# Optimization experiments

Hardware: AMD Instinct MI355X
Metric: run time of the kernel (lower is better)

The kernel has to match this reference:

```python
import jax, jax.numpy as jnp
import numpy as np

# --- hyperparameters (from MambaBlock init) ---
DIM = 256          # d_model per window
STEP = 128         # int(dim * hop), hop = 0.5
N_MAMBA = 2
D_STATE = 16
D_CONV = 4
EXPAND = 4
D_INNER = EXPAND * DIM          # 1024
DT_RANK = -(-DIM // 16)         # ceil(d_model/16) = 16
EPS = 1e-5
B_SZ = 4
T_LEN = 131072


def setup_inputs() -> dict:
    key = jax.random.key(0)
    ks = jax.random.split(key, 8)
    s = 0.02
    x = jax.random.normal(ks[0], (B_SZ, T_LEN), dtype=jnp.float32)
    in_proj_w = jax.random.normal(ks[1], (N_MAMBA, 2 * D_INNER, DIM), dtype=jnp.float32) * s
    conv_w = jax.random.normal(ks[2], (N_MAMBA, D_INNER, 1, D_CONV), dtype=jnp.float32) * 0.1
    conv_b = jnp.zeros((N_MAMBA, D_INNER), dtype=jnp.float32)
    x_proj_w = jax.random.normal(ks[3], (N_MAMBA, DT_RANK + 2 * D_STATE, D_INNER), dtype=jnp.float32) * s
    dt_std = DT_RANK ** -0.5
    dt_proj_w = jax.random.uniform(ks[4], (N_MAMBA, D_INNER, DT_RANK), minval=-dt_std, maxval=dt_std, dtype=jnp.float32)
    # dt bias: inverse-softplus of dt ~ LogUniform[1e-3, 0.1] (mamba_ssm init)
    dt = jnp.exp(jax.random.uniform(ks[5], (N_MAMBA, D_INNER), dtype=jnp.float32)
                 * (np.log(0.1) - np.log(1e-3)) + np.log(1e-3))
    dt_proj_b = dt + jnp.log(-jnp.expm1(-dt))
    A_log = jnp.log(jnp.broadcast_to(jnp.arange(1, D_STATE + 1, dtype=jnp.float32),
                                     (N_MAMBA, D_INNER, D_STATE)))
    D_param = jnp.ones((N_MAMBA, D_INNER), dtype=jnp.float32)
    out_proj_w = jax.random.normal(ks[6], (N_MAMBA, DIM, D_INNER), dtype=jnp.float32) * s
    norm_w = jnp.ones((N_MAMBA, DIM), dtype=jnp.float32)
    return dict(x=x, in_proj_w=in_proj_w, conv_w=conv_w, conv_b=conv_b,
                x_proj_w=x_proj_w, dt_proj_w=dt_proj_w, dt_proj_b=dt_proj_b,
                A_log=A_log, D_param=D_param, out_proj_w=out_proj_w, norm_w=norm_w)


def _rmsnorm(x, w):
    return x * jax.lax.rsqrt(jnp.mean(x * x, axis=-1, keepdims=True) + EPS) * w


def _selective_scan(u, delta, A, Bm, Cm, Dp):
    # u, delta: [B, L, Di]; A: [Di, N]; Bm, Cm: [B, L, N]; Dp: [Di]
    def step(h, inp):
        u_t, d_t, B_t, C_t = inp                       # [B,Di],[B,Di],[B,N],[B,N]
        dA = jnp.exp(d_t[:, :, None] * A)              # [B,Di,N]
        h = dA * h + (d_t * u_t)[:, :, None] * B_t[:, None, :]
        y_t = jnp.einsum('bdn,bn->bd', h, C_t)
        return h, y_t
    h0 = jnp.zeros((u.shape[0], u.shape[2], A.shape[1]), u.dtype)
    xs = (u.transpose(1, 0, 2), delta.transpose(1, 0, 2),
          Bm.transpose(1, 0, 2), Cm.transpose(1, 0, 2))
    _, ys = jax.lax.scan(step, h0, xs)                 # ys: [L, B, Di]
    return ys.transpose(1, 0, 2) + u * Dp


def _mamba(x, in_w, cw, cb, xp_w, dt_w, dt_b, A_log, Dp, out_w):
    # x: [B, L, d_model]
    xz = jnp.einsum('bld,ed->ble', x, in_w)            # [B, L, 2*Di]
    xc, z = jnp.split(xz, 2, axis=-1)
    # causal depthwise conv (torch pads d_conv-1 both sides then truncates to L)
    xc = xc.transpose(0, 2, 1)                         # [B, Di, L]
    xc = jax.lax.conv_general_dilated(xc, cw, window_strides=(1,),
                                      padding=[(D_CONV - 1, 0)],
                                      feature_group_count=D_INNER,
                                      dimension_numbers=('NCH', 'OIH', 'NCH'))
    xc = jax.nn.silu(xc + cb[None, :, None]).transpose(0, 2, 1)  # [B, L, Di]
    x_dbl = jnp.einsum('bld,ed->ble', xc, xp_w)        # [B, L, dt_rank + 2N]
    dt = x_dbl[..., :DT_RANK]
    Bm = x_dbl[..., DT_RANK:DT_RANK + D_STATE]
    Cm = x_dbl[..., DT_RANK + D_STATE:]
    delta = jax.nn.softplus(jnp.einsum('blr,dr->bld', dt, dt_w) + dt_b)
    A = -jnp.exp(A_log)                                # [Di, N]
    y = _selective_scan(xc, delta, A, Bm, Cm, Dp)
    y = y * jax.nn.silu(z)
    return jnp.einsum('bld,ed->ble', y, out_w)         # [B, L, d_model]


def _forward(x, in_proj_w, conv_w, conv_b, x_proj_w, dt_proj_w, dt_proj_b,
             A_log, D_param, out_proj_w, norm_w):
    B, T = x.shape
    L = (T - DIM) // STEP + 1
    idx = jnp.arange(L)[:, None] * STEP + jnp.arange(DIM)[None, :]  # [L, DIM]
    h = x[:, idx]                                      # unfold -> [B, L, DIM]
    res = None
    for i in range(N_MAMBA):
        res = h + res if res is not None else h        # Block residual chaining
        hn = _rmsnorm(res, norm_w[i])
        h = _mamba(hn, in_proj_w[i], conv_w[i], conv_b[i], x_proj_w[i],
                   dt_proj_w[i], dt_proj_b[i], A_log[i], D_param[i], out_proj_w[i])
    r = h + res
    # hop < 1: triangular window, then fold (overlap-add)
    half = DIM // 2
    win = jnp.concatenate([jnp.linspace(0.0, 1.0, half), jnp.linspace(1.0, 0.0, half)])
    r = r * win
    folded = jnp.zeros_like(x).at[:, idx].add(r)       # F.fold overlap-add
    return folded + x


def reference(x, in_proj_w, conv_w, conv_b, x_proj_w, dt_proj_w, dt_proj_b,
              A_log, D_param, out_proj_w, norm_w):
    return _forward(x, in_proj_w, conv_w, conv_b, x_proj_w, dt_proj_w, dt_proj_b,
                    A_log, D_param, out_proj_w, norm_w)
```

## Files before the change

kernel.cpp:

```cpp
#include <hip/hip_runtime.h>
#include <cmath>

#define DIMC   256
#define L_WIN  1023
#define M_VALID 4092
#define M_PAD  4096
#define DI     1024
#define TLEN   131072
#define SEG    32
#define NSEG   32

typedef __bf16 bf16x8 __attribute__((ext_vector_type(8)));
typedef __bf16 bf16x4 __attribute__((ext_vector_type(4)));
typedef float  f32x4  __attribute__((ext_vector_type(4)));

__device__ __forceinline__ float sigmoidf_(float x){ return 1.f/(1.f + __expf(-x)); }
__device__ __forceinline__ float softplusf_(float v){ return fmaxf(v,0.f) + log1pf(__expf(-fabsf(v))); }

template<int CTRL>
__device__ __forceinline__ float dpp_add(float x){
  int v = __builtin_amdgcn_update_dpp(0, __builtin_bit_cast(int, x), CTRL, 0xF, 0xF, true);
  return x + __builtin_bit_cast(float, v);
}

__global__ __launch_bounds__(256) void init_kernel(const float* __restrict__ x, float* __restrict__ res,
    const float* __restrict__ a, __bf16* __restrict__ da, int na,
    const float* __restrict__ b, __bf16* __restrict__ db, int nb,
    const float* __restrict__ c, __bf16* __restrict__ dc, int nc)
{
  if (blockIdx.x < M_PAD){
    int m = blockIdx.x, j = threadIdx.x;
    float v = 0.f;
    if (m < M_VALID){
      int bb = m / L_WIN, l = m - bb*L_WIN;
      v = x[(size_t)bb*TLEN + l*128 + j];
    }
    res[(size_t)m*DIMC + j] = v;
    return;
  }
  int nblk = gridDim.x - M_PAD;
  int stride = nblk*256;
  int base = (blockIdx.x - M_PAD)*256 + threadIdx.x;
  for (int i = base; i < na; i += stride) da[i] = (__bf16)a[i];
  for (int i = base; i < nb; i += stride) db[i] = (__bf16)b[i];
  for (int i = base; i < nc; i += stride) dc[i] = (__bf16)c[i];
}

__global__ __launch_bounds__(256) void rms_kernel(const float* __restrict__ src, __bf16* __restrict__ dst,
                                                  const float* __restrict__ w){
  int m = blockIdx.x, j = threadIdx.x;
  float v = (m < M_VALID) ? src[(size_t)m*DIMC + j] : 0.f;
  float s = v*v;
  #pragma unroll
  for (int off = 32; off; off >>= 1) s += __shfl_down(s, off);
  __shared__ float ls[4];
  if ((threadIdx.x & 63) == 0) ls[threadIdx.x >> 6] = s;
  __syncthreads();
  float tot = ls[0] + ls[1] + ls[2] + ls[3];
  float scale = rsqrtf(tot * (1.f/DIMC) + 1e-5f);
  dst[(size_t)m*DIMC + j] = (__bf16)(v * scale * w[j]);
}

template<int WM, int WN, typename OutT>
__global__ __launch_bounds__(256) void gemm_tiled_kernel(const __bf16* __restrict__ A, const __bf16* __restrict__ B,
    OutT* C, const float* addsrc, int K, int ldc)
{
  constexpr int BM  = 32*WM;
  constexpr int BN  = 32*WN;
  constexpr int LDK = 72;
  __shared__ __bf16 As[BM*LDK];
  __shared__ __bf16 Bs[BN*LDK];
  int tid  = threadIdx.x;
  int lane = tid & 63, wv = tid >> 6;
  int row  = lane & 15, kq = lane >> 4;
  int m0 = blockIdx.x*BM, n0 = blockIdx.y*BN;
  int wmo = (wv >> 1)*(16*WM);
  int wno = (wv &  1)*(16*WN);
  f32x4 acc[WM][WN] = {};
  for (int kt = 0; kt < K; kt += 64){
    __syncthreads();
    #pragma unroll
    for (int r = 0; r < BM/32; ++r){
      int seg = r*256 + tid;
      int rw = seg >> 3, sb = seg & 7;
      *(bf16x8*)(As + rw*LDK + sb*8) = *(const bf16x8*)(A + (size_t)(m0 + rw)*K + kt + sb*8);
    }
    #pragma unroll
    for (int r = 0; r < BN/32; ++r){
      int seg = r*256 + tid;
      int rw = seg >> 3, sb = seg & 7;
      *(bf16x8*)(Bs + rw*LDK + sb*8) = *(const bf16x8*)(B + (size_t)(n0 + rw)*K + kt + sb*8);
    }
    __syncthreads();
    #pragma unroll
    for (int ks = 0; ks < 2; ++ks){
      bf16x8 af[WM], bfr[WN];
      #pragma unroll
      for (int i = 0; i < WM; ++i) af[i]  = *(const bf16x8*)(As + (wmo + i*16 + row)*LDK + ks*32 + kq*8);
      #pragma unroll
      for (int j = 0; j < WN; ++j) bfr[j] = *(const bf16x8*)(Bs + (wno + j*16 + row)*LDK + ks*32 + kq*8);
      #pragma unroll
      for (int i = 0; i < WM; ++i){
        #pragma unroll
        for (int j = 0; j < WN; ++j)
          acc[i][j] = __builtin_amdgcn_mfma_f32_16x16x32_bf16(af[i], bfr[j], acc[i][j], 0, 0, 0);
      }
    }
  }
  #pragma unroll
  for (int i = 0; i < WM; ++i){
    int cm = m0 + wmo + i*16 + kq*4;
    #pragma unroll
    for (int j = 0; j < WN; ++j){
      int cn = n0 + wno + j*16 + row;
      #pragma unroll
      for (int ii = 0; ii < 4; ++ii){
        size_t idx = (size_t)(cm + ii)*ldc + cn;
        float v = acc[i][j][ii];
        if (addsrc) v += addsrc[idx];
        C[idx] = (OutT)v;
      }
    }
  }
}

__global__ __launch_bounds__(256) void conv_xproj_dt_kernel(
  const __bf16* __restrict__ xz16, const float* __restrict__ cw, const float* __restrict__ cb,
  const __bf16* __restrict__ wxp, const float* __restrict__ dtw, const float* __restrict__ dtb,
  __bf16* __restrict__ u16, float* __restrict__ xdbl, __bf16* __restrict__ delta16)
{
  __shared__ __bf16 su[16][1032];
  __shared__ float  sdt[16][17];
  int tid = threadIdx.x;
  int m0 = blockIdx.x * 16;
  {
    int d = tid * 4;
    float w[4][4], bias[4];
    #pragma unroll
    for (int c = 0; c < 4; ++c){
      #pragma unroll
      for (int j = 0; j < 4; ++j) w[c][j] = cw[(d + c)*4 + j];
      bias[c] = cb[d + c];
    }
    for (int ti = 0; ti < 16; ++ti){
      int m = m0 + ti;
      float acc[4] = {0.f, 0.f, 0.f, 0.f};
      if (m < M_VALID){
        int b = m / L_WIN;
        int l = m - b*L_WIN;
        #pragma unroll
        for (int c = 0; c < 4; ++c) acc[c] = bias[c];
        #pragma unroll
        for (int k = 0; k < 4; ++k){
          if (l >= k){
            bf16x4 xv = *(const bf16x4*)(xz16 + (size_t)(m - k)*2048 + d);
            #pragma unroll
            for (int c = 0; c < 4; ++c) acc[c] = fmaf((float)xv[c], w[c][3-k], acc[c]);
          }
        }
        #pragma unroll
        for (int c = 0; c < 4; ++c) acc[c] = acc[c] * sigmoidf_(acc[c]);
      }
      bf16x4 o;
      #pragma unroll
      for (int c = 0; c < 4; ++c) o[c] = (__bf16)acc[c];
      *(bf16x4*)(u16 + (size_t)m*DI + d) = o;
      *(bf16x4*)(&su[ti][d]) = o;
    }
  }
  __syncthreads();
  {
    int lane = tid & 63, wv = tid >> 6;
    if (wv < 3){
      int row = lane & 15, kq = lane >> 4;
      f32x4 acc = {0.f, 0.f, 0.f, 0.f};
      const __bf16* Bp = wxp + (size_t)(wv*16 + row)*1024 + kq*8;
      for (int k = 0; k < 1024; k += 32){
        bf16x8 a  = *(const bf16x8*)(&su[row][k + kq*8]);
        bf16x8 bb = *(const bf16x8*)(Bp + k);
        acc = __builtin_amdgcn_mfma_f32_16x16x32_bf16(a, bb, acc, 0, 0, 0);
      }
      #pragma unroll
      for (int i = 0; i < 4; ++i){
        int tok = kq*4 + i;
        xdbl[(size_t)(m0 + tok)*48 + wv*16 + row] = acc[i];
        if (wv == 0) sdt[tok][row] = acc[i];
      }
    }
  }
  __syncthreads();
  {
    int d0 = tid * 4;
    float w[4][16], bias[4];
    #pragma unroll
    for (int c = 0; c < 4; ++c){
      #pragma unroll
      for (int q = 0; q < 16; ++q) w[c][q] = dtw[(d0 + c)*16 + q];
      bias[c] = dtb[d0 + c];
    }
    for (int t = 0; t < 16; ++t){
      float acc[4] = {bias[0], bias[1], bias[2], bias[3]};
      #pragma unroll
      for (int r = 0; r < 16; ++r){
        float dv = sdt[t][r];
        #pragma unroll
        for (int c = 0; c < 4; ++c) acc[c] = fmaf(dv, w[c][r], acc[c]);
      }
      bf16x4 o;
      #pragma unroll
      for (int c = 0; c < 4; ++c) o[c] = (__bf16)softplusf_(acc[c]);
      *(bf16x4*)(delta16 + (size_t)(m0 + t)*DI + d0) = o;
    }
  }
}

__global__ __launch_bounds__(256) void scan_part1_kernel(
  const __bf16* __restrict__ u16, const __bf16* __restrict__ delta16,
  const float* __restrict__ xdbl, const float* __restrict__ Alog, float2* __restrict__ Pq)
{
  int bid = blockIdx.x;
  int s = bid & 31, dtile = (bid >> 5) & 63, b = bid >> 11;
  int d0 = dtile << 4;
  int tid = threadIdx.x;
  int c = tid >> 4, n = tid & 15;
  float A_dn = -__expf(Alog[(d0 + c)*16 + n]);
  __shared__ float2 sdd[16][SEG+2];
  __shared__ float  sB [SEG][17];
  int t0 = s*SEG;
  int nt = L_WIN - t0; if (nt > SEG) nt = SEG;
  size_t base_m = (size_t)b*L_WIN + t0;
  for (int i2 = tid; i2 < 16*SEG; i2 += 256){
    int tt = i2 >> 4, dd = i2 & 15;
    float dlt = 0.f, du = 0.f, Bv = 0.f;
    if (tt < nt){
      size_t m = base_m + tt;
      dlt = (float)delta16[m*DI + d0 + dd];
      du  = dlt * (float)u16[m*DI + d0 + dd];
      Bv  = xdbl[m*48 + 16 + dd];
    }
    sdd[dd][tt] = make_float2(dlt, du);
    sB[tt][dd]  = Bv;
  }
  __syncthreads();
  float h = 0.f, P = 1.f;
  #pragma unroll 8
  for (int t = 0; t < SEG; ++t){
    float2 dd2 = sdd[c][t];
    float dA = __expf(dd2.x * A_dn);
    h = fmaf(dA, h, dd2.y * sB[t][n]);
    P *= dA;
  }
  Pq[(((size_t)b*NSEG + s) << 14) + d0*16 + tid] = make_float2(P, h);
}

__global__ __launch_bounds__(256) void scan_combine_kernel(const float2* __restrict__ Pq,
                                                           float* __restrict__ hstart)
{
  int idx = blockIdx.x*256 + threadIdx.x;
  int b = idx >> 14;
  int dn = idx & 16383;
  float hs = 0.f;
  #pragma unroll
  for (int s = 0; s < NSEG; ++s){
    size_t o = (((size_t)b*NSEG + s) << 14) + dn;
    hstart[o] = hs;
    float2 pq = Pq[o];
    hs = fmaf(pq.x, hs, pq.y);
  }
}

__global__ __launch_bounds__(256) void scan_part2_kernel(
  const __bf16* __restrict__ u16, const __bf16* __restrict__ delta16,
  const float* __restrict__ xdbl, const __bf16* __restrict__ xz16,
  const float* __restrict__ Alog, const float* __restrict__ Dp,
  const float* __restrict__ hstart, __bf16* __restrict__ y16)
{
  int bid = blockIdx.x;
  int s = bid & 31, dtile = (bid >> 5) & 63, b = bid >> 11;
  int d0 = dtile << 4;
  int tid = threadIdx.x;
  int c = tid >> 4, n = tid & 15;
  float A_dn = -__expf(Alog[(d0 + c)*16 + n]);
  __shared__ float2 sdd[16][SEG+2];
  __shared__ float2 sBC[SEG][17];
  __shared__ float  sy [16][SEG+1];
  __shared__ float  sD[16];
  if (tid < 16) sD[tid] = Dp[d0 + tid];
  int t0 = s*SEG;
  int nt = L_WIN - t0; if (nt > SEG) nt = SEG;
  size_t base_m = (size_t)b*L_WIN + t0;
  for (int i2 = tid; i2 < 16*SEG; i2 += 256){
    int tt = i2 >> 4, dd = i2 & 15;
    float dlt = 0.f, uu = 0.f, Bv = 0.f, Cv = 0.f;
    if (tt < nt){
      size_t m = base_m + tt;
      dlt = (float)delta16[m*DI + d0 + dd];
      uu  = (float)u16[m*DI + d0 + dd];
      Bv  = xdbl[m*48 + 16 + dd];
      Cv  = xdbl[m*48 + 32 + dd];
    }
    sdd[dd][tt] = make_float2(dlt, uu);
    sBC[tt][dd] = make_float2(Bv, Cv);
  }
  float h = hstart[(((size_t)b*NSEG + s) << 14) + d0*16 + tid];
  __syncthreads();
  #pragma unroll 8
  for (int t = 0; t < SEG; ++t){
    float2 dd2 = sdd[c][t];
    float dA = __expf(dd2.x * A_dn);
    float2 bc = sBC[t][n];
    h = fmaf(dA, h, dd2.x * dd2.y * bc.x);
    float pp = h * bc.y;
    pp = dpp_add<0xB1>(pp);
    pp = dpp_add<0x4E>(pp);
    pp = dpp_add<0x141>(pp);
    pp = dpp_add<0x128>(pp);
    if (n == 0) sy[c][t] = pp;
  }
  __syncthreads();
  for (int i2 = tid; i2 < 16*nt; i2 += 256){
    int tt = i2 >> 4, dd = i2 & 15;
    size_t m = base_m + tt;
    float uv = sdd[dd][tt].y;
    float zv = (float)xz16[m*2048 + 1024 + d0 + dd];
    float yv = (sy[dd][tt] + uv * sD[dd]) * (zv * sigmoidf_(zv));
    y16[m*DI + d0 + dd] = (__bf16)yv;
  }
}

__global__ __launch_bounds__(256) void fold_kernel(const float* __restrict__ x, const float* __restrict__ r,
                                                   float* __restrict__ out){
  int i = blockIdx.x*256 + threadIdx.x;
  int b = i >> 17;
  int t = i & (TLEN - 1);
  float acc = x[i];
  int l1 = t >> 7;
  int j  = t & 127;
  if (l1 < L_WIN) acc += r[((size_t)b*L_WIN + l1)*DIMC + j] * ((float)j * (1.f/127.f));
  if (l1 >= 1)    acc += r[((size_t)b*L_WIN + l1 - 1)*DIMC + j + 128] * ((float)(127 - j) * (1.f/127.f));
  out[i] = acc;
}

extern "C" void kernel_launch(void* const* d_in, const int* in_sizes, int n_in,
                              void* d_out, int out_size, void* d_ws, size_t ws_size,
                              hipStream_t stream)
{
  (void)in_sizes; (void)n_in; (void)out_size; (void)ws_size;
  const float* x      = (const float*)d_in[0];
  const float* in_w   = (const float*)d_in[1];
  const float* conv_w = (const float*)d_in[2];
  const float* conv_b = (const float*)d_in[3];
  const float* xp_w   = (const float*)d_in[4];
  const float* dt_w   = (const float*)d_in[5];
  const float* dt_b   = (const float*)d_in[6];
  const float* A_log  = (const float*)d_in[7];
  const float* Dp     = (const float*)d_in[8];
  const float* out_w  = (const float*)d_in[9];
  const float* norm_w = (const float*)d_in[10];
  float* out = (float*)d_out;

  char* p = (char*)d_ws;
  auto alloc = [&](size_t bytes)->void*{ void* r = (void*)p; p += (bytes + 255) & ~(size_t)255; return r; };
  float*  res    = (float*) alloc((size_t)M_PAD*DIMC*4);
  __bf16* hn16   = (__bf16*)alloc((size_t)M_PAD*DIMC*2);
  __bf16* xz16   = (__bf16*)alloc((size_t)M_PAD*2048*2);
  __bf16* u16    = (__bf16*)alloc((size_t)M_PAD*DI*2);
  float*  xdbl   = (float*) alloc((size_t)M_PAD*48*4);
  __bf16* delta16= (__bf16*)alloc((size_t)M_PAD*DI*2);
  __bf16* y16    = (__bf16*)alloc((size_t)M_PAD*DI*2);
  float2* Pq     = (float2*)alloc((size_t)4*NSEG*16384*8);
  float*  hstart = (float*) alloc((size_t)4*NSEG*16384*4);
  __bf16* w_in16 = (__bf16*)alloc((size_t)2*2048*256*2);
  __bf16* w_xp16 = (__bf16*)alloc((size_t)2*48*1024*2);
  __bf16* w_out16= (__bf16*)alloc((size_t)2*256*1024*2);

  init_kernel<<<M_PAD + 512, 256, 0, stream>>>(x, res,
                                               in_w, w_in16, 2*2048*256,
                                               xp_w, w_xp16, 2*48*1024,
                                               out_w, w_out16, 2*256*1024);

  for (int i = 0; i < 2; ++i){
    rms_kernel<<<M_PAD, 256, 0, stream>>>(res, hn16, norm_w + i*256);
    gemm_tiled_kernel<4, 4, __bf16><<<dim3(32, 16), 256, 0, stream>>>(hn16, w_in16 + (size_t)i*524288, xz16, nullptr, 256, 2048);
    conv_xproj_dt_kernel<<<M_PAD/16, 256, 0, stream>>>(xz16, conv_w + i*4096, conv_b + i*1024,
                                                       w_xp16 + (size_t)i*49152, dt_w + i*16384, dt_b + i*1024,
                                                       u16, xdbl, delta16);
    scan_part1_kernel<<<8192, 256, 0, stream>>>(u16, delta16, xdbl, A_log + i*16384, Pq);
    scan_combine_kernel<<<256, 256, 0, stream>>>(Pq, hstart);
    scan_part2_kernel<<<8192, 256, 0, stream>>>(u16, delta16, xdbl, xz16, A_log + i*16384, Dp + i*1024,
                                                hstart, y16);
    gemm_tiled_kernel<2, 2, float><<<dim3(64, 4), 256, 0, stream>>>(y16, w_out16 + (size_t)i*262144, res, res, 1024, 256);
  }
  fold_kernel<<<TLEN*4/256, 256, 0, stream>>>(x, res, out);
}
```

Measured before the change: 339.4 us.

## Store scan inputs in d-tile-major permuted layout for contiguous scan loads

The in-projection GEMM now splits its output into a conv input buffer and a z buffer laid out per 16-channel tile. The conv/xproj kernel writes u and delta in the same tile-major layout and packs B and C as interleaved float2. Both scan kernels can then read each segment's tile as contiguous runs instead of 32-byte strided slices of 1024-wide rows. The cost is extra permuted-store scatter in the producer kernels, whose z stores in the GEMM epilogue are 2-byte scattered writes.

New measurement: 344.9 us. About the same (+1.6%).

```diff
diff --git a/kernel.cpp b/kernel.cpp
--- a/kernel.cpp
+++ b/kernel.cpp
@@ -9,9 +9,11 @@
 #define TLEN   131072
 #define SEG    32
 #define NSEG   32
+#define DTSTRIDE 65536
 
 typedef __bf16 bf16x8 __attribute__((ext_vector_type(8)));
 typedef __bf16 bf16x4 __attribute__((ext_vector_type(4)));
+typedef __bf16 bf16x2 __attribute__((ext_vector_type(2)));
 typedef float  f32x4  __attribute__((ext_vector_type(4)));
 
 __device__ __forceinline__ float sigmoidf_(float x){ return 1.f/(1.f + __expf(-x)); }
@@ -61,32 +63,93 @@
   dst[(size_t)m*DIMC + j] = (__bf16)(v * scale * w[j]);
 }
 
-template<int WM, int WN, typename OutT>
-__global__ __launch_bounds__(256) void gemm_tiled_kernel(const __bf16* __restrict__ A, const __bf16* __restrict__ B,
-    OutT* C, const float* addsrc, int K, int ldc)
-{
-  constexpr int BM  = 32*WM;
-  constexpr int BN  = 32*WN;
+__global__ __launch_bounds__(256) void gemm_inproj_kernel(const __bf16* __restrict__ A, const __bf16* __restrict__ B,
+    __bf16* __restrict__ xc16, __bf16* __restrict__ z_perm)
+{
   constexpr int LDK = 72;
-  __shared__ __bf16 As[BM*LDK];
-  __shared__ __bf16 Bs[BN*LDK];
+  __shared__ __bf16 As[128*LDK];
+  __shared__ __bf16 Bs[128*LDK];
   int tid  = threadIdx.x;
   int lane = tid & 63, wv = tid >> 6;
   int row  = lane & 15, kq = lane >> 4;
-  int m0 = blockIdx.x*BM, n0 = blockIdx.y*BN;
-  int wmo = (wv >> 1)*(16*WM);
-  int wno = (wv &  1)*(16*WN);
-  f32x4 acc[WM][WN] = {};
+  int m0 = blockIdx.x*128, n0 = blockIdx.y*128;
+  int wmo = (wv >> 1)*64;
+  int wno = (wv &  1)*64;
+  f32x4 acc[4][4] = {};
+  for (int kt = 0; kt < 256; kt += 64){
+    __syncthreads();
+    #pragma unroll
+    for (int r = 0; r < 4; ++r){
+      int seg = r*256 + tid;
+      int rw = seg >> 3, sb = seg & 7;
+      *(bf16x8*)(As + rw*LDK + sb*8) = *(const bf16x8*)(A + (size_t)(m0 + rw)*256 + kt + sb*8);
+    }
+    #pragma unroll
+    for (int r = 0; r < 4; ++r){
+      int seg = r*256 + tid;
+      int rw = seg >> 3, sb = seg & 7;
+      *(bf16x8*)(Bs + rw*LDK + sb*8) = *(const bf16x8*)(B + (size_t)(n0 + rw)*256 + kt + sb*8);
+    }
+    __syncthreads();
+    #pragma unroll
+    for (int ks = 0; ks < 2; ++ks){
+      bf16x8 af[4], bfr[4];
+      #pragma unroll
+      for (int i = 0; i < 4; ++i) af[i]  = *(const bf16x8*)(As + (wmo + i*16 + row)*LDK + ks*32 + kq*8);
+      #pragma unroll
+      for (int j = 0; j < 4; ++j) bfr[j] = *(const bf16x8*)(Bs + (wno + j*16 + row)*LDK + ks*32 + kq*8);
+      #pragma unroll
+      for (int i = 0; i < 4; ++i){
+        #pragma unroll
+        for (int j = 0; j < 4; ++j)
+          acc[i][j] = __builtin_amdgcn_mfma_f32_16x16x32_bf16(af[i], bfr[j], acc[i][j], 0, 0, 0);
+      }
+    }
+  }
+  bool isz = (n0 >= 1024);
+  #pragma unroll
+  for (int i = 0; i < 4; ++i){
+    int cm = m0 + wmo + i*16 + kq*4;
+    #pragma unroll
+    for (int j = 0; j < 4; ++j){
+      int cn = n0 + wno + j*16 + row;
+      #pragma unroll
+      for (int ii = 0; ii < 4; ++ii){
+        __bf16 bv = (__bf16)acc[i][j][ii];
+        if (!isz){
+          xc16[(size_t)(cm + ii)*1024 + cn] = bv;
+        } else {
+          int zn = cn - 1024;
+          z_perm[(size_t)(zn >> 4)*DTSTRIDE + (size_t)(cm + ii)*16 + (zn & 15)] = bv;
+        }
+      }
+    }
+  }
+}
+
+__global__ __launch_bounds__(256) void gemm_outproj_kernel(const __bf16* __restrict__ A, const __bf16* __restrict__ B,
+    float* C, int K, int ldc)
+{
+  constexpr int LDK = 72;
+  __shared__ __bf16 As[64*LDK];
+  __shared__ __bf16 Bs[64*LDK];
+  int tid  = threadIdx.x;
+  int lane = tid & 63, wv = tid >> 6;
+  int row  = lane & 15, kq = lane >> 4;
+  int m0 = blockIdx.x*64, n0 = blockIdx.y*64;
+  int wmo = (wv >> 1)*32;
+  int wno = (wv &  1)*32;
+  f32x4 acc[2][2] = {};
   for (int kt = 0; kt < K; kt += 64){
     __syncthreads();
     #pragma unroll
-    for (int r = 0; r < BM/32; ++r){
+    for (int r = 0; r < 2; ++r){
       int seg = r*256 + tid;
       int rw = seg >> 3, sb = seg & 7;
       *(bf16x8*)(As + rw*LDK + sb*8) = *(const bf16x8*)(A + (size_t)(m0 + rw)*K + kt + sb*8);
     }
     #pragma unroll
-    for (int r = 0; r < BN/32; ++r){
+    for (int r = 0; r < 2; ++r){
       int seg = r*256 + tid;
       int rw = seg >> 3, sb = seg & 7;
       *(bf16x8*)(Bs + rw*LDK + sb*8) = *(const bf16x8*)(B + (size_t)(n0 + rw)*K + kt + sb*8);
@@ -94,40 +157,38 @@
     __syncthreads();
     #pragma unroll
     for (int ks = 0; ks < 2; ++ks){
-      bf16x8 af[WM], bfr[WN];
-      #pragma unroll
-      for (int i = 0; i < WM; ++i) af[i]  = *(const bf16x8*)(As + (wmo + i*16 + row)*LDK + ks*32 + kq*8);
-      #pragma unroll
-      for (int j = 0; j < WN; ++j) bfr[j] = *(const bf16x8*)(Bs + (wno + j*16 + row)*LDK + ks*32 + kq*8);
-      #pragma unroll
-      for (int i = 0; i < WM; ++i){
-        #pragma unroll
-        for (int j = 0; j < WN; ++j)
+      bf16x8 af[2], bfr[2];
+      #pragma unroll
+      for (int i = 0; i < 2; ++i) af[i]  = *(const bf16x8*)(As + (wmo + i*16 + row)*LDK + ks*32 + kq*8);
+      #pragma unroll
+      for (int j = 0; j < 2; ++j) bfr[j] = *(const bf16x8*)(Bs + (wno + j*16 + row)*LDK + ks*32 + kq*8);
+      #pragma unroll
+      for (int i = 0; i < 2; ++i){
+        #pragma unroll
+        for (int j = 0; j < 2; ++j)
           acc[i][j] = __builtin_amdgcn_mfma_f32_16x16x32_bf16(af[i], bfr[j], acc[i][j], 0, 0, 0);
       }
     }
   }
   #pragma unroll
-  for (int i = 0; i < WM; ++i){
+  for (int i = 0; i < 2; ++i){
     int cm = m0 + wmo + i*16 + kq*4;
     #pragma unroll
-    for (int j = 0; j < WN; ++j){
+    for (int j = 0; j < 2; ++j){
       int cn = n0 + wno + j*16 + row;
       #pragma unroll
       for (int ii = 0; ii < 4; ++ii){
         size_t idx = (size_t)(cm + ii)*ldc + cn;
-        float v = acc[i][j][ii];
-        if (addsrc) v += addsrc[idx];
-        C[idx] = (OutT)v;
+        C[idx] = C[idx] + acc[i][j][ii];
       }
     }
   }
 }
 
 __global__ __launch_bounds__(256) void conv_xproj_dt_kernel(
-  const __bf16* __restrict__ xz16, const float* __restrict__ cw, const float* __restrict__ cb,
+  const __bf16* __restrict__ xc16, const float* __restrict__ cw, const float* __restrict__ cb,
   const __bf16* __restrict__ wxp, const float* __restrict__ dtw, const float* __restrict__ dtb,
-  __bf16* __restrict__ u16, float* __restrict__ xdbl, __bf16* __restrict__ delta16)
+  __bf16* __restrict__ u_perm, float2* __restrict__ BCp, __bf16* __restrict__ delta_perm)
 {
   __shared__ __bf16 su[16][1032];
   __shared__ float  sdt[16][17];
@@ -153,7 +214,7 @@
         #pragma unroll
         for (int k = 0; k < 4; ++k){
           if (l >= k){
-            bf16x4 xv = *(const bf16x4*)(xz16 + (size_t)(m - k)*2048 + d);
+            bf16x4 xv = *(const bf16x4*)(xc16 + (size_t)(m - k)*1024 + d);
             #pragma unroll
             for (int c = 0; c < 4; ++c) acc[c] = fmaf((float)xv[c], w[c][3-k], acc[c]);
           }
@@ -164,11 +225,18 @@
       bf16x4 o;
       #pragma unroll
       for (int c = 0; c < 4; ++c) o[c] = (__bf16)acc[c];
-      *(bf16x4*)(u16 + (size_t)m*DI + d) = o;
       *(bf16x4*)(&su[ti][d]) = o;
     }
   }
   __syncthreads();
+  #pragma unroll
+  for (int it = 0; it < 4; ++it){
+    int idx = it*256 + tid;
+    int dtile = idx >> 4, ti = idx & 15;
+    const bf16x8* s = (const bf16x8*)(&su[ti][dtile*16]);
+    bf16x8* dpp = (bf16x8*)(u_perm + (size_t)dtile*DTSTRIDE + (size_t)(m0 + ti)*16);
+    dpp[0] = s[0]; dpp[1] = s[1];
+  }
   {
     int lane = tid & 63, wv = tid >> 6;
     if (wv < 3){
@@ -183,14 +251,16 @@
       #pragma unroll
       for (int i = 0; i < 4; ++i){
         int tok = kq*4 + i;
-        xdbl[(size_t)(m0 + tok)*48 + wv*16 + row] = acc[i];
         if (wv == 0) sdt[tok][row] = acc[i];
+        else if (wv == 1) BCp[(size_t)(m0 + tok)*16 + row].x = acc[i];
+        else              BCp[(size_t)(m0 + tok)*16 + row].y = acc[i];
       }
     }
   }
   __syncthreads();
   {
     int d0 = tid * 4;
+    int dtile = tid >> 2, dd = (tid & 3)*4;
     float w[4][16], bias[4];
     #pragma unroll
     for (int c = 0; c < 4; ++c){
@@ -209,14 +279,14 @@
       bf16x4 o;
       #pragma unroll
       for (int c = 0; c < 4; ++c) o[c] = (__bf16)softplusf_(acc[c]);
-      *(bf16x4*)(delta16 + (size_t)(m0 + t)*DI + d0) = o;
+      *(bf16x4*)(delta_perm + (size_t)dtile*DTSTRIDE + (size_t)(m0 + t)*16 + dd) = o;
     }
   }
 }
 
 __global__ __launch_bounds__(256) void scan_part1_kernel(
-  const __bf16* __restrict__ u16, const __bf16* __restrict__ delta16,
-  const float* __restrict__ xdbl, const float* __restrict__ Alog, float2* __restrict__ Pq)
+  const __bf16* __restrict__ u_perm, const __bf16* __restrict__ delta_perm,
+  const float2* __restrict__ BCp, const float* __restrict__ Alog, float2* __restrict__ Pq)
 {
   int bid = blockIdx.x;
   int s = bid & 31, dtile = (bid >> 5) & 63, b = bid >> 11;
@@ -229,17 +299,21 @@
   int t0 = s*SEG;
   int nt = L_WIN - t0; if (nt > SEG) nt = SEG;
   size_t base_m = (size_t)b*L_WIN + t0;
-  for (int i2 = tid; i2 < 16*SEG; i2 += 256){
-    int tt = i2 >> 4, dd = i2 & 15;
-    float dlt = 0.f, du = 0.f, Bv = 0.f;
+  {
+    int tt = tid >> 3, nn = (tid & 7)*2;
+    float dl0=0.f, dl1=0.f, du0=0.f, du1=0.f, B0=0.f, B1=0.f;
     if (tt < nt){
-      size_t m = base_m + tt;
-      dlt = (float)delta16[m*DI + d0 + dd];
-      du  = dlt * (float)u16[m*DI + d0 + dd];
-      Bv  = xdbl[m*48 + 16 + dd];
-    }
-    sdd[dd][tt] = make_float2(dlt, du);
-    sB[tt][dd]  = Bv;
+      size_t mrow = base_m + tt;
+      bf16x2 d2 = *(const bf16x2*)(delta_perm + (size_t)dtile*DTSTRIDE + mrow*16 + nn);
+      bf16x2 u2 = *(const bf16x2*)(u_perm     + (size_t)dtile*DTSTRIDE + mrow*16 + nn);
+      f32x4 bc  = *(const f32x4*)(BCp + mrow*16 + nn);
+      dl0 = (float)d2[0]; dl1 = (float)d2[1];
+      du0 = dl0*(float)u2[0]; du1 = dl1*(float)u2[1];
+      B0 = bc.x; B1 = bc.z;
+    }
+    sdd[nn][tt]   = make_float2(dl0, du0);
+    sdd[nn+1][tt] = make_float2(dl1, du1);
+    sB[tt][nn] = B0; sB[tt][nn+1] = B1;
   }
   __syncthreads();
   float h = 0.f, P = 1.f;
@@ -270,8 +344,8 @@
 }
 
 __global__ __launch_bounds__(256) void scan_part2_kernel(
-  const __bf16* __restrict__ u16, const __bf16* __restrict__ delta16,
-  const float* __restrict__ xdbl, const __bf16* __restrict__ xz16,
+  const __bf16* __restrict__ u_perm, const __bf16* __restrict__ delta_perm,
+  const float2* __restrict__ BCp, const __bf16* __restrict__ z_perm,
   const float* __restrict__ Alog, const float* __restrict__ Dp,
   const float* __restrict__ hstart, __bf16* __restrict__ y16)
 {
@@ -289,18 +363,21 @@
   int t0 = s*SEG;
   int nt = L_WIN - t0; if (nt > SEG) nt = SEG;
   size_t base_m = (size_t)b*L_WIN + t0;
-  for (int i2 = tid; i2 < 16*SEG; i2 += 256){
-    int tt = i2 >> 4, dd = i2 & 15;
-    float dlt = 0.f, uu = 0.f, Bv = 0.f, Cv = 0.f;
+  int tt = tid >> 3, nn = (tid & 7)*2;
+  {
+    float dl0=0.f, dl1=0.f, u0=0.f, u1=0.f;
+    f32x4 bc = {0.f, 0.f, 0.f, 0.f};
     if (tt < nt){
-      size_t m = base_m + tt;
-      dlt = (float)delta16[m*DI + d0 + dd];
-      uu  = (float)u16[m*DI + d0 + dd];
-      Bv  = xdbl[m*48 + 16 + dd];
-      Cv  = xdbl[m*48 + 32 + dd];
-    }
-    sdd[dd][tt] = make_float2(dlt, uu);
-    sBC[tt][dd] = make_float2(Bv, Cv);
+      size_t mrow = base_m + tt;
+      bf16x2 d2 = *(const bf16x2*)(delta_perm + (size_t)dtile*DTSTRIDE + mrow*16 + nn);
+      bf16x2 u2 = *(const bf16x2*)(u_perm     + (size_t)dtile*DTSTRIDE + mrow*16 + nn);
+      bc = *(const f32x4*)(BCp + mrow*16 + nn);
+      dl0 = (float)d2[0]; dl1 = (float)d2[1];
+      u0 = (float)u2[0];  u1 = (float)u2[1];
+    }
+    sdd[nn][tt]   = make_float2(dl0, u0);
+    sdd[nn+1][tt] = make_float2(dl1, u1);
+    *(f32x4*)(&sBC[tt][nn]) = bc;
   }
   float h = hstart[(((size_t)b*NSEG + s) << 14) + d0*16 + tid];
   __syncthreads();
@@ -318,13 +395,19 @@
     if (n == 0) sy[c][t] = pp;
   }
   __syncthreads();
-  for (int i2 = tid; i2 < 16*nt; i2 += 256){
-    int tt = i2 >> 4, dd = i2 & 15;
-    size_t m = base_m + tt;
-    float uv = sdd[dd][tt].y;
-    float zv = (float)xz16[m*2048 + 1024 + d0 + dd];
-    float yv = (sy[dd][tt] + uv * sD[dd]) * (zv * sigmoidf_(zv));
-    y16[m*DI + d0 + dd] = (__bf16)yv;
+  if (tt < nt){
+    size_t mrow = base_m + tt;
+    bf16x2 z2 = *(const bf16x2*)(z_perm + (size_t)dtile*DTSTRIDE + mrow*16 + nn);
+    bf16x2 o;
+    #pragma unroll
+    for (int c2 = 0; c2 < 2; ++c2){
+      int dd = nn + c2;
+      float uv = sdd[dd][tt].y;
+      float zv = (float)z2[c2];
+      float yv = (sy[dd][tt] + uv * sD[dd]) * (zv * sigmoidf_(zv));
+      o[c2] = (__bf16)yv;
+    }
+    *(bf16x2*)(y16 + mrow*DI + d0 + nn) = o;
   }
 }
 
@@ -361,18 +444,19 @@
 
   char* p = (char*)d_ws;
   auto alloc = [&](size_t bytes)->void*{ void* r = (void*)p; p += (bytes + 255) & ~(size_t)255; return r; };
-  float*  res    = (float*) alloc((size_t)M_PAD*DIMC*4);
-  __bf16* hn16   = (__bf16*)alloc((size_t)M_PAD*DIMC*2);
-  __bf16* xz16   = (__bf16*)alloc((size_t)M_PAD*2048*2);
-  __bf16* u16    = (__bf16*)alloc((size_t)M_PAD*DI*2);
-  float*  xdbl   = (float*) alloc((size_t)M_PAD*48*4);
-  __bf16* delta16= (__bf16*)alloc((size_t)M_PAD*DI*2);
-  __bf16* y16    = (__bf16*)alloc((size_t)M_PAD*DI*2);
-  float2* Pq     = (float2*)alloc((size_t)4*NSEG*16384*8);
-  float*  hstart = (float*) alloc((size_t)4*NSEG*16384*4);
-  __bf16* w_in16 = (__bf16*)alloc((size_t)2*2048*256*2);
-  __bf16* w_xp16 = (__bf16*)alloc((size_t)2*48*1024*2);
-  __bf16* w_out16= (__bf16*)alloc((size_t)2*256*1024*2);
+  float*  res     = (float*) alloc((size_t)M_PAD*DIMC*4);
+  __bf16* hn16    = (__bf16*)alloc((size_t)M_PAD*DIMC*2);
+  __bf16* xc16    = (__bf16*)alloc((size_t)M_PAD*1024*2);
+  __bf16* z_perm  = (__bf16*)alloc((size_t)64*DTSTRIDE*2);
+  __bf16* u_perm  = (__bf16*)alloc((size_t)64*DTSTRIDE*2);
+  __bf16* delta_perm = (__bf16*)alloc((size_t)64*DTSTRIDE*2);
+  float2* BCp     = (float2*)alloc((size_t)M_PAD*16*8);
+  __bf16* y16     = (__bf16*)alloc((size_t)M_PAD*DI*2);
+  float2* Pq      = (float2*)alloc((size_t)4*NSEG*16384*8);
+  float*  hstart  = (float*) alloc((size_t)4*NSEG*16384*4);
+  __bf16* w_in16  = (__bf16*)alloc((size_t)2*2048*256*2);
+  __bf16* w_xp16  = (__bf16*)alloc((size_t)2*48*1024*2);
+  __bf16* w_out16 = (__bf16*)alloc((size_t)2*256*1024*2);
 
   init_kernel<<<M_PAD + 512, 256, 0, stream>>>(x, res,
                                                in_w, w_in16, 2*2048*256,
@@ -381,15 +465,15 @@
 
   for (int i = 0; i < 2; ++i){
     rms_kernel<<<M_PAD, 256, 0, stream>>>(res, hn16, norm_w + i*256);
-    gemm_tiled_kernel<4, 4, __bf16><<<dim3(32, 16), 256, 0, stream>>>(hn16, w_in16 + (size_t)i*524288, xz16, nullptr, 256, 2048);
-    conv_xproj_dt_kernel<<<M_PAD/16, 256, 0, stream>>>(xz16, conv_w + i*4096, conv_b + i*1024,
+    gemm_inproj_kernel<<<dim3(32, 16), 256, 0, stream>>>(hn16, w_in16 + (size_t)i*524288, xc16, z_perm);
+    conv_xproj_dt_kernel<<<M_PAD/16, 256, 0, stream>>>(xc16, conv_w + i*4096, conv_b + i*1024,
                                                        w_xp16 + (size_t)i*49152, dt_w + i*16384, dt_b + i*1024,
-                                                       u16, xdbl, delta16);
-    scan_part1_kernel<<<8192, 256, 0, stream>>>(u16, delta16, xdbl, A_log + i*16384, Pq);
+                                                       u_perm, BCp, delta_perm);
+    scan_part1_kernel<<<8192, 256, 0, stream>>>(u_perm, delta_perm, BCp, A_log + i*16384, Pq);
     scan_combine_kernel<<<256, 256, 0, stream>>>(Pq, hstart);
-    scan_part2_kernel<<<8192, 256, 0, stream>>>(u16, delta16, xdbl, xz16, A_log + i*16384, Dp + i*1024,
+    scan_part2_kernel<<<8192, 256, 0, stream>>>(u_perm, delta_perm, BCp, z_perm, A_log + i*16384, Dp + i*1024,
                                                 hstart, y16);
-    gemm_tiled_kernel<2, 2, float><<<dim3(64, 4), 256, 0, stream>>>(y16, w_out16 + (size_t)i*262144, res, res, 1024, 256);
+    gemm_outproj_kernel<<<dim3(64, 4), 256, 0, stream>>>(y16, w_out16 + (size_t)i*262144, res, 1024, 256);
   }
   fold_kernel<<<TLEN*4/256, 256, 0, stream>>>(x, res, out);
 }
```
